# Performance work log

Hardware: AMD Instinct MI355X
Metric: run time of the kernel (lower is better)

The kernel has to match this reference:

```python
import jax, jax.numpy as jnp
import numpy as np

DIM = 256
MUL = 4
NUM_ENTRIES = 64
B, K = 16, 64
R = MUL * DIM


def setup_inputs() -> dict:
    key = jax.random.key(0)
    k_slots, k_idx, k_w1, k_w2 = jax.random.split(key, 4)
    slots = jax.random.normal(k_slots, (B, K, DIM), dtype=jnp.float32)
    indices = jax.random.randint(k_idx, (B, K), 0, NUM_ENTRIES, dtype=jnp.int64)
    # xavier_normal: std = sqrt(2 / (fan_in + fan_out)) over last two dims
    std1 = float(np.sqrt(2.0 / (DIM + R)))
    std2 = float(np.sqrt(2.0 / (R + DIM)))
    w1 = jax.random.normal(k_w1, (NUM_ENTRIES, DIM, R), dtype=jnp.float32) * std1
    w2 = jax.random.normal(k_w2, (NUM_ENTRIES, R, DIM), dtype=jnp.float32) * std2
    b1 = jnp.zeros((NUM_ENTRIES, R), dtype=jnp.float32)
    b2 = jnp.zeros((NUM_ENTRIES, DIM), dtype=jnp.float32)
    return {"slots": slots, "w1": w1, "b1": b1, "w2": w2, "b2": b2, "indices": indices}


def reference(slots, w1, b1, w2, b2, indices):
    # gather per-(b,k) expert weights, then 2-layer MLP (matvec per slot)
    h = jnp.einsum('bkd,bkdr->bkr', slots, w1[indices]) + b1[indices]  # (B,K,R)
    h = jax.nn.relu(h)
    out = jnp.einsum('bkr,bkrd->bkd', h, w2[indices]) + b2[indices]    # (B,K,DIM)
    return out
```

## Files before the change

### kernel.cpp

```cpp
#include <hip/hip_runtime.h>
#include <stdint.h>

#define DIMC 256
#define RTOT 1024
#define NE 64
#define NSLOT 1024
#define RCN 8
#define RCW 128
#define TILE 32
#define XSTR 264
#define KS1 8
#define KS2 4
#define NTW2 2

typedef short bfrag __attribute__((ext_vector_type(8)));
typedef float f32x4 __attribute__((ext_vector_type(4)));

__global__ __launch_bounds__(1024) void bucket_kernel(
    const int* __restrict__ idx, int* __restrict__ count,
    int* __restrict__ start, int* __restrict__ list) {
  __shared__ int cnt[NE];
  __shared__ int offs[NE];
  __shared__ int cur[NE];
  int t = threadIdx.x;
  if (t < NE) cnt[t] = 0;
  __syncthreads();
  int e = idx[t] & (NE - 1);
  atomicAdd(&cnt[e], 1);
  __syncthreads();
  if (t == 0) {
    int acc = 0;
    for (int i = 0; i < NE; ++i) { offs[i] = acc; cur[i] = acc; acc += cnt[i]; }
  }
  __syncthreads();
  if (t < NE) { count[t] = cnt[t]; start[t] = offs[t]; }
  int pos = atomicAdd(&cur[e], 1);
  list[pos] = t;
}

static __device__ __forceinline__ unsigned short f2bf(float f) {
  unsigned u = __float_as_uint(f);
  return (unsigned short)((u + 0x7FFFu + ((u >> 16) & 1u)) >> 16);
}

static __device__ __forceinline__ bfrag pack8(const float* f) {
  union { unsigned short u[8]; bfrag v; } r;
#pragma unroll
  for (int i = 0; i < 8; ++i) r.u[i] = f2bf(f[i]);
  return r.v;
}

__global__ __launch_bounds__(512) void mlp_kernel(
    const float* __restrict__ slots, const float* __restrict__ w1,
    const float* __restrict__ b1, const float* __restrict__ w2,
    const float* __restrict__ b2, const int* __restrict__ count,
    const int* __restrict__ start, const int* __restrict__ list,
    float* __restrict__ out) {
  const int rc = blockIdx.x;
  const int e  = blockIdx.y;
  const int n  = count[e];
  if (n == 0) return;
  const int t  = threadIdx.x;
  const int l  = t & 63;
  const int w  = t >> 6;
  const int ln = l & 15;
  const int kg = l >> 4;
  const int rbase = rc * RCW;
  const int st = start[e];

  __shared__ unsigned short X[TILE * XSTR];
  __shared__ int sid[TILE];

  const float* w1e = w1 + (size_t)e * DIMC * RTOT + rbase;
  const float* w2e = w2 + (size_t)e * RTOT * DIMC + (size_t)rbase * DIMC;

  for (int s0 = 0; s0 < n; s0 += TILE) {
    const int m = (n - s0 < TILE) ? (n - s0) : TILE;

    __syncthreads();
    if (t < TILE) sid[t] = (t < m) ? list[st + s0 + t] : 0;
    __syncthreads();

    for (int i = t; i < TILE * 64; i += 512) {
      int s = i >> 6, d4 = (i & 63) * 4;
      float4 v = make_float4(0.f, 0.f, 0.f, 0.f);
      if (s < m) v = ((const float4*)slots)[(size_t)sid[s] * 64 + (i & 63)];
      union { unsigned short u[4]; uint2 q; } p;
      p.u[0] = f2bf(v.x); p.u[1] = f2bf(v.y);
      p.u[2] = f2bf(v.z); p.u[3] = f2bf(v.w);
      *(uint2*)&X[s * XSTR + d4] = p.q;
    }
    __syncthreads();

    f32x4 acc1[2];
    acc1[0] = (f32x4)(0.f); acc1[1] = (f32x4)(0.f);
    {
      const int col = w * 16 + ln;
      float bc[8], bn[8];
#pragma unroll
      for (int j = 0; j < 8; ++j)
        bc[j] = w1e[(size_t)(kg * 8 + j) * RTOT + col];

#pragma unroll
      for (int ks = 0; ks < KS1; ++ks) {
        if (ks + 1 < KS1) {
          const int kb = (ks + 1) * 32;
#pragma unroll
          for (int j = 0; j < 8; ++j)
            bn[j] = w1e[(size_t)(kb + kg * 8 + j) * RTOT + col];
        }
        const unsigned short* xp = &X[(size_t)ln * XSTR + ks * 32 + kg * 8];
        bfrag a0 = *(const bfrag*)xp;
        bfrag a1 = *(const bfrag*)(xp + 16 * XSTR);
        bfrag b = pack8(bc);
        acc1[0] = __builtin_amdgcn_mfma_f32_16x16x32_bf16(a0, b, acc1[0], 0, 0, 0);
        acc1[1] = __builtin_amdgcn_mfma_f32_16x16x32_bf16(a1, b, acc1[1], 0, 0, 0);
#pragma unroll
        for (int j = 0; j < 8; ++j) bc[j] = bn[j];
      }
    }

    __syncthreads();

    {
      const int col = w * 16 + ln;
      const float b1v = b1[e * RTOT + rbase + col];
#pragma unroll
      for (int mt = 0; mt < 2; ++mt)
#pragma unroll
        for (int reg = 0; reg < 4; ++reg) {
          float h = fmaxf(acc1[mt][reg] + b1v, 0.f);
          X[(mt * 16 + kg * 4 + reg) * XSTR + col] = f2bf(h);
        }
    }
    __syncthreads();

    f32x4 acc2[2][NTW2];
#pragma unroll
    for (int mt = 0; mt < 2; ++mt)
#pragma unroll
      for (int nt = 0; nt < NTW2; ++nt) acc2[mt][nt] = (f32x4)(0.f);
    {
      float bc[NTW2][8], bn[NTW2][8];
#pragma unroll
      for (int nt = 0; nt < NTW2; ++nt)
#pragma unroll
        for (int j = 0; j < 8; ++j)
          bc[nt][j] = w2e[(size_t)(kg * 8 + j) * DIMC + w * 32 + nt * 16 + ln];

#pragma unroll
      for (int ks = 0; ks < KS2; ++ks) {
        if (ks + 1 < KS2) {
          const int kb = (ks + 1) * 32;
#pragma unroll
          for (int nt = 0; nt < NTW2; ++nt)
#pragma unroll
            for (int j = 0; j < 8; ++j)
              bn[nt][j] = w2e[(size_t)(kb + kg * 8 + j) * DIMC + w * 32 + nt * 16 + ln];
        }
        const unsigned short* xp = &X[(size_t)ln * XSTR + ks * 32 + kg * 8];
        bfrag a0 = *(const bfrag*)xp;
        bfrag a1 = *(const bfrag*)(xp + 16 * XSTR);
#pragma unroll
        for (int nt = 0; nt < NTW2; ++nt) {
          bfrag b = pack8(bc[nt]);
          acc2[0][nt] = __builtin_amdgcn_mfma_f32_16x16x32_bf16(a0, b, acc2[0][nt], 0, 0, 0);
          acc2[1][nt] = __builtin_amdgcn_mfma_f32_16x16x32_bf16(a1, b, acc2[1][nt], 0, 0, 0);
        }
#pragma unroll
        for (int nt = 0; nt < NTW2; ++nt)
#pragma unroll
          for (int j = 0; j < 8; ++j) bc[nt][j] = bn[nt][j];
      }
    }

#pragma unroll
    for (int nt = 0; nt < NTW2; ++nt) {
      const int col = w * 32 + nt * 16 + ln;
      const float b2v = (rc == 0) ? b2[e * DIMC + col] : 0.f;
#pragma unroll
      for (int mt = 0; mt < 2; ++mt)
#pragma unroll
        for (int reg = 0; reg < 4; ++reg) {
          const int row = mt * 16 + kg * 4 + reg;
          if (row < m)
            atomicAdd(&out[(size_t)sid[row] * DIMC + col], acc2[mt][nt][reg] + b2v);
        }
    }
  }
}

extern "C" void kernel_launch(void* const* d_in, const int* in_sizes, int n_in,
                              void* d_out, int out_size, void* d_ws, size_t ws_size,
                              hipStream_t stream) {
  const float* slots   = (const float*)d_in[0];
  const float* w1      = (const float*)d_in[1];
  const float* b1      = (const float*)d_in[2];
  const float* w2      = (const float*)d_in[3];
  const float* b2      = (const float*)d_in[4];
  const int*   indices = (const int*)d_in[5];
  float* out = (float*)d_out;

  int* ws    = (int*)d_ws;
  int* count = ws;
  int* start = ws + 64;
  int* list  = ws + 128;

  hipMemsetAsync(d_out, 0, (size_t)out_size * sizeof(float), stream);
  bucket_kernel<<<1, NSLOT, 0, stream>>>(indices, count, start, list);
  mlp_kernel<<<dim3(RCN, NE), 512, 0, stream>>>(slots, w1, b1, w2, b2,
                                                count, start, list, out);
}
```

Before: 171.4 us.

## Stream weight tiles into LDS via async global_load_lds triple buffering

Replaces per-thread register prefetch of w1/w2 columns with async direct-to-LDS loads (global_load_lds) into a three-slot shared buffer, running both layers as one 16-step pipelined tile loop. The aim is to overlap weight fetches with MFMA work and to issue wide coalesced 16-byte loads instead of strided scalar loads. It adds 48KB of LDS, which may lower occupancy, and a block-wide barrier on every tile step.

Measured after the change: 177.8 us. 3.7% more time.

```diff
diff --git a/kernel.cpp b/kernel.cpp
--- a/kernel.cpp
+++ b/kernel.cpp
@@ -9,12 +9,12 @@
 #define RCW 128
 #define TILE 32
 #define XSTR 264
-#define KS1 8
-#define KS2 4
-#define NTW2 2
+#define NTILE 16
 
 typedef short bfrag __attribute__((ext_vector_type(8)));
 typedef float f32x4 __attribute__((ext_vector_type(4)));
+typedef const __attribute__((address_space(1))) void* gptr_t;
+typedef __attribute__((address_space(3))) void* lptr_t;
 
 __global__ __launch_bounds__(1024) void bucket_kernel(
     const int* __restrict__ idx, int* __restrict__ count,
@@ -50,6 +50,21 @@
   return r.v;
 }
 
+static __device__ __forceinline__ void dma_tile(
+    const float* __restrict__ src, int row_stride, int row_shift, int col_mask,
+    float* slot, int w, int l) {
+#pragma unroll
+  for (int i = 0; i < 2; ++i) {
+    const int base = (i * 8 + w) * 256;
+    const int f = base + l * 4;
+    const int row = f >> row_shift;
+    const int col = f & col_mask;
+    __builtin_amdgcn_global_load_lds(
+        (gptr_t)(src + (size_t)row * row_stride + col),
+        (lptr_t)(slot + base), 16, 0, 0);
+  }
+}
+
 __global__ __launch_bounds__(512) void mlp_kernel(
     const float* __restrict__ slots, const float* __restrict__ w1,
     const float* __restrict__ b1, const float* __restrict__ w2,
@@ -68,6 +83,7 @@
   const int rbase = rc * RCW;
   const int st = start[e];
 
+  __shared__ float wbuf[3][4096];
   __shared__ unsigned short X[TILE * XSTR];
   __shared__ int sid[TILE];
 
@@ -81,6 +97,7 @@
     if (t < TILE) sid[t] = (t < m) ? list[st + s0 + t] : 0;
     __syncthreads();
 
+    dma_tile(w1e, RTOT, 7, 127, wbuf[0], w, l);
     for (int i = t; i < TILE * 64; i += 512) {
       int s = i >> 6, d4 = (i & 63) * 4;
       float4 v = make_float4(0.f, 0.f, 0.f, 0.f);
@@ -94,88 +111,73 @@
 
     f32x4 acc1[2];
     acc1[0] = (f32x4)(0.f); acc1[1] = (f32x4)(0.f);
-    {
-      const int col = w * 16 + ln;
-      float bc[8], bn[8];
-#pragma unroll
-      for (int j = 0; j < 8; ++j)
-        bc[j] = w1e[(size_t)(kg * 8 + j) * RTOT + col];
-
-#pragma unroll
-      for (int ks = 0; ks < KS1; ++ks) {
-        if (ks + 1 < KS1) {
-          const int kb = (ks + 1) * 32;
-#pragma unroll
-          for (int j = 0; j < 8; ++j)
-            bn[j] = w1e[(size_t)(kb + kg * 8 + j) * RTOT + col];
-        }
-        const unsigned short* xp = &X[(size_t)ln * XSTR + ks * 32 + kg * 8];
+    f32x4 acc2[2][2];
+
+    for (int tk = 0; tk < NTILE; ++tk) {
+      if (tk + 1 < NTILE) {
+        const int kn = tk + 1;
+        if (kn < 8)
+          dma_tile(w1e + (size_t)(32 * kn) * RTOT, RTOT, 7, 127,
+                   wbuf[kn % 3], w, l);
+        else
+          dma_tile(w2e + (size_t)(16 * (kn - 8)) * DIMC, DIMC, 8, 255,
+                   wbuf[kn % 3], w, l);
+      }
+
+      if (tk < 8) {
+        const float* B = wbuf[tk % 3];
+        const int col = w * 16 + ln;
+        float bv[8];
+#pragma unroll
+        for (int j = 0; j < 8; ++j) bv[j] = B[(kg * 8 + j) * 128 + col];
+        bfrag b = pack8(bv);
+        const unsigned short* xp = &X[(size_t)ln * XSTR + tk * 32 + kg * 8];
         bfrag a0 = *(const bfrag*)xp;
         bfrag a1 = *(const bfrag*)(xp + 16 * XSTR);
-        bfrag b = pack8(bc);
         acc1[0] = __builtin_amdgcn_mfma_f32_16x16x32_bf16(a0, b, acc1[0], 0, 0, 0);
         acc1[1] = __builtin_amdgcn_mfma_f32_16x16x32_bf16(a1, b, acc1[1], 0, 0, 0);
-#pragma unroll
-        for (int j = 0; j < 8; ++j) bc[j] = bn[j];
-      }
-    }
-
-    __syncthreads();
-
-    {
-      const int col = w * 16 + ln;
-      const float b1v = b1[e * RTOT + rbase + col];
-#pragma unroll
-      for (int mt = 0; mt < 2; ++mt)
-#pragma unroll
-        for (int reg = 0; reg < 4; ++reg) {
-          float h = fmaxf(acc1[mt][reg] + b1v, 0.f);
-          X[(mt * 16 + kg * 4 + reg) * XSTR + col] = f2bf(h);
+
+        if (tk == 7) {
+          __syncthreads();
+          const float b1v = b1[e * RTOT + rbase + col];
+#pragma unroll
+          for (int mt = 0; mt < 2; ++mt) {
+#pragma unroll
+            for (int reg = 0; reg < 4; ++reg) {
+              float h = fmaxf(acc1[mt][reg] + b1v, 0.f);
+              X[(mt * 16 + kg * 4 + reg) * XSTR + col] = f2bf(h);
+            }
+          }
+#pragma unroll
+          for (int mt = 0; mt < 2; ++mt)
+#pragma unroll
+            for (int nt = 0; nt < 2; ++nt) acc2[mt][nt] = (f32x4)(0.f);
         }
-    }
-    __syncthreads();
-
-    f32x4 acc2[2][NTW2];
-#pragma unroll
-    for (int mt = 0; mt < 2; ++mt)
-#pragma unroll
-      for (int nt = 0; nt < NTW2; ++nt) acc2[mt][nt] = (f32x4)(0.f);
-    {
-      float bc[NTW2][8], bn[NTW2][8];
-#pragma unroll
-      for (int nt = 0; nt < NTW2; ++nt)
-#pragma unroll
-        for (int j = 0; j < 8; ++j)
-          bc[nt][j] = w2e[(size_t)(kg * 8 + j) * DIMC + w * 32 + nt * 16 + ln];
-
-#pragma unroll
-      for (int ks = 0; ks < KS2; ++ks) {
-        if (ks + 1 < KS2) {
-          const int kb = (ks + 1) * 32;
-#pragma unroll
-          for (int nt = 0; nt < NTW2; ++nt)
-#pragma unroll
-            for (int j = 0; j < 8; ++j)
-              bn[nt][j] = w2e[(size_t)(kb + kg * 8 + j) * DIMC + w * 32 + nt * 16 + ln];
-        }
-        const unsigned short* xp = &X[(size_t)ln * XSTR + ks * 32 + kg * 8];
+      } else if (tk & 1) {
+        const int ks2 = (tk - 9) >> 1;
+        const float* Be = wbuf[(tk - 1) % 3];
+        const float* Bo = wbuf[tk % 3];
+        const float* Bk = (kg & 2) ? Bo : Be;
+        const int krow = (kg & 1) * 8;
+        const unsigned short* xp = &X[(size_t)ln * XSTR + ks2 * 32 + kg * 8];
         bfrag a0 = *(const bfrag*)xp;
         bfrag a1 = *(const bfrag*)(xp + 16 * XSTR);
 #pragma unroll
-        for (int nt = 0; nt < NTW2; ++nt) {
-          bfrag b = pack8(bc[nt]);
+        for (int nt = 0; nt < 2; ++nt) {
+          const int col = w * 32 + nt * 16 + ln;
+          float bv[8];
+#pragma unroll
+          for (int j = 0; j < 8; ++j) bv[j] = Bk[(krow + j) * 256 + col];
+          bfrag b = pack8(bv);
           acc2[0][nt] = __builtin_amdgcn_mfma_f32_16x16x32_bf16(a0, b, acc2[0][nt], 0, 0, 0);
           acc2[1][nt] = __builtin_amdgcn_mfma_f32_16x16x32_bf16(a1, b, acc2[1][nt], 0, 0, 0);
         }
-#pragma unroll
-        for (int nt = 0; nt < NTW2; ++nt)
-#pragma unroll
-          for (int j = 0; j < 8; ++j) bc[nt][j] = bn[nt][j];
       }
+      __syncthreads();
     }
 
 #pragma unroll
-    for (int nt = 0; nt < NTW2; ++nt) {
+    for (int nt = 0; nt < 2; ++nt) {
       const int col = w * 32 + nt * 16 + ln;
       const float b2v = (rc == 0) ? b2[e * DIMC + col] : 0.f;
 #pragma unroll
@@ -187,6 +189,8 @@
             atomicAdd(&out[(size_t)sid[row] * DIMC + col], acc2[mt][nt][reg] + b2v);
         }
     }
+
+    acc1[0] = (f32x4)(0.f); acc1[1] = (f32x4)(0.f);
   }
 }
 
```
